# Optimization experiments

Hardware: AMD Instinct MI355X
Metric: run time of the kernel (lower is better)

Reference implementation:

```python
import jax, jax.numpy as jnp
import numpy as np

HID = 16

def _lrconv(x, edge_index, edge_attr, w1, b1, w2, b2):
    # flow='target_to_source': x_i = x[edge_index[0]], x_j = x[edge_index[1]],
    # aggregate (max) at edge_index[0].
    src = edge_index[0]
    dst = edge_index[1]
    m = jnp.concatenate([x[src], x[dst], edge_attr], axis=-1)  # [E, 2*in+edge]
    m = jax.nn.relu(m @ w1 + b1)
    m = jax.nn.relu(m @ w2 + b2)  # [E, out], all >= 0
    agg = jax.ops.segment_max(m, src, num_segments=x.shape[0])
    # empty segments get -inf in jax; PyG fills with 0. Messages are ReLU'd (>=0),
    # so clamping at 0 is exact.
    return jnp.maximum(agg, 0.0)

def _glorot(key, shape):
    fan_in, fan_out = shape
    lim = float(np.sqrt(6.0 / (fan_in + fan_out)))
    return jax.random.uniform(key, shape, jnp.float32, -lim, lim)

def setup_inputs() -> dict:
    key = jax.random.key(0)
    ks = jax.random.split(key, 16)
    N, E = 100000, 1600000
    x = jax.random.normal(ks[0], (N, 4), jnp.float32)
    edge_index = jax.random.randint(ks[1], (2, E), 0, N, jnp.int64)
    edge_attr = jax.random.normal(ks[2], (E, 8), jnp.float32)
    # conv1: in=4 -> cat dim 4*2+8=16
    c1_w1 = _glorot(ks[3], (16, HID)); c1_b1 = jnp.zeros((HID,), jnp.float32)
    c1_w2 = _glorot(ks[4], (HID, 16)); c1_b2 = jnp.zeros((16,), jnp.float32)
    # conv2: in=16 -> cat dim 16*2+8=40
    c2_w1 = _glorot(ks[5], (40, HID)); c2_b1 = jnp.zeros((HID,), jnp.float32)
    c2_w2 = _glorot(ks[6], (HID, 16)); c2_b2 = jnp.zeros((16,), jnp.float32)
    l1_w = _glorot(ks[7], (16, 16)); l1_b = jnp.zeros((16,), jnp.float32)
    l2_w = _glorot(ks[8], (16, 1)); l2_b = jnp.zeros((1,), jnp.float32)
    return {"x": x, "edge_index": edge_index, "edge_attr": edge_attr,
            "c1_w1": c1_w1, "c1_b1": c1_b1, "c1_w2": c1_w2, "c1_b2": c1_b2,
            "c2_w1": c2_w1, "c2_b1": c2_b1, "c2_w2": c2_w2, "c2_b2": c2_b2,
            "l1_w": l1_w, "l1_b": l1_b, "l2_w": l2_w, "l2_b": l2_b}

def reference(x, edge_index, edge_attr,
              c1_w1, c1_b1, c1_w2, c1_b2,
              c2_w1, c2_b1, c2_w2, c2_b2,
              l1_w, l1_b, l2_w, l2_b):
    h = _lrconv(x, edge_index, edge_attr, c1_w1, c1_b1, c1_w2, c1_b2)   # [N,16]
    h = _lrconv(h, edge_index, edge_attr, c2_w1, c2_b1, c2_w2, c2_b2)   # [N,16]
    h = jax.nn.relu(h @ l1_w + l1_b)
    return h @ l2_w + l2_b  # [N,1]
```

## Files before the change

kernel.cpp:

```cpp
#include <hip/hip_runtime.h>
#include <hip/hip_fp16.h>

#define CHUNK 1024
#define NBKT 4

typedef _Float16 half8 __attribute__((ext_vector_type(8)));
typedef float floatx4 __attribute__((ext_vector_type(4)));

__device__ __forceinline__ unsigned int pack2(float a, float b) {
    __half2 h = __floats2half2_rn(a, b);
    return *(unsigned int*)&h;
}
__device__ __forceinline__ float2 unpack2(unsigned int u) {
    __half2 h = *(__half2*)&u;
    return __half22float2(h);
}

__global__ __launch_bounds__(256) void rank_cvt(
    const int* __restrict__ ei, const float* __restrict__ ea,
    int* __restrict__ deg, unsigned short* __restrict__ r,
    _Float16* __restrict__ eah, int E)
{
    int e = blockIdx.x * 256 + threadIdx.x;
    if (e >= E) return;
    int bkt = (e >> 8) & (NBKT - 1);
    r[e] = (unsigned short)atomicAdd(&deg[(size_t)ei[e] * NBKT + bkt], 1);
    float4 a0 = *(const float4*)(ea + (size_t)e * 8);
    float4 a1 = *(const float4*)(ea + (size_t)e * 8 + 4);
    half8 h;
    h[0] = (_Float16)a0.x; h[1] = (_Float16)a0.y;
    h[2] = (_Float16)a0.z; h[3] = (_Float16)a0.w;
    h[4] = (_Float16)a1.x; h[5] = (_Float16)a1.y;
    h[6] = (_Float16)a1.z; h[7] = (_Float16)a1.w;
    *(half8*)(eah + (size_t)e * 8) = h;
}

__global__ __launch_bounds__(256) void scan_chunk_sums(
    const int* __restrict__ v, int* __restrict__ csum, int N)
{
    __shared__ int s[256];
    int base = blockIdx.x * CHUNK;
    int t = threadIdx.x;
    int acc = 0;
    #pragma unroll
    for (int i = 0; i < CHUNK / 256; ++i) {
        int idx = base + t + i * 256;
        if (idx < N) acc += v[idx];
    }
    s[t] = acc; __syncthreads();
    for (int o = 128; o > 0; o >>= 1) {
        if (t < o) s[t] += s[t + o];
        __syncthreads();
    }
    if (t == 0) csum[blockIdx.x] = s[0];
}

__global__ __launch_bounds__(256) void scan_chunk_off(
    const int* __restrict__ csum, int* __restrict__ coff, int nch)
{
    __shared__ int s[256];
    __shared__ int carry;
    int t = threadIdx.x;
    if (t == 0) carry = 0;
    __syncthreads();
    for (int base = 0; base < nch; base += 256) {
        int v = (base + t < nch) ? csum[base + t] : 0;
        s[t] = v; __syncthreads();
        for (int o = 1; o < 256; o <<= 1) {
            int add = (t >= o) ? s[t - o] : 0;
            __syncthreads();
            s[t] += add;
            __syncthreads();
        }
        int excl = carry + (t > 0 ? s[t - 1] : 0);
        if (base + t < nch) coff[base + t] = excl;
        __syncthreads();
        if (t == 0) carry += s[255];
        __syncthreads();
    }
}

__global__ __launch_bounds__(256) void scan_within_excl(
    const int* __restrict__ deg, int* __restrict__ pos,
    const int* __restrict__ coff, int N)
{
    __shared__ int s[256];
    int t = threadIdx.x;
    int base = blockIdx.x * CHUNK + t * 4;
    int v0 = 0, v1 = 0, v2 = 0, v3 = 0;
    if (base + 0 < N) v0 = deg[base + 0];
    if (base + 1 < N) v1 = deg[base + 1];
    if (base + 2 < N) v2 = deg[base + 2];
    if (base + 3 < N) v3 = deg[base + 3];
    s[t] = v0 + v1 + v2 + v3;
    __syncthreads();
    for (int o = 1; o < 256; o <<= 1) {
        int add = (t >= o) ? s[t - o] : 0;
        __syncthreads();
        s[t] += add;
        __syncthreads();
    }
    int run = coff[blockIdx.x] + (t > 0 ? s[t - 1] : 0);
    if (base + 0 < N) pos[base + 0] = run; run += v0;
    if (base + 1 < N) pos[base + 1] = run; run += v1;
    if (base + 2 < N) pos[base + 2] = run; run += v2;
    if (base + 3 < N) pos[base + 3] = run;
}

__global__ __launch_bounds__(256) void edge_mlp1(
    const float* __restrict__ x,
    const int*   __restrict__ ei,
    const _Float16* __restrict__ eah,
    const int*   __restrict__ pos,
    const unsigned short* __restrict__ r,
    const float* __restrict__ w1, const float* __restrict__ b1,
    const float* __restrict__ w2, const float* __restrict__ b2,
    _Float16* __restrict__ m2h,
    int E)
{
    __shared__ _Float16 itm[4][4][16][24];
    int tid = threadIdx.x;
    int w = tid >> 6, lane = tid & 63;
    int e16 = lane & 15, q = lane >> 4;
    int ntiles = (E + 63) >> 6;
    int tile = blockIdx.x * 4 + w;
    if (tile >= ntiles) return;
    int ebase = tile << 6;
    int e = ebase + lane;

    int s_l = 0, d_l = 0, p_l = 0;
    if (e < E) {
        s_l = ei[e];
        d_l = ei[E + e];
        p_l = pos[(size_t)s_l * NBKT + ((e >> 8) & (NBKT - 1))] + (int)r[e];
    }

    half8 B1, B2;
    #pragma unroll
    for (int j = 0; j < 8; ++j) { B1[j] = (_Float16)0.f; B2[j] = (_Float16)0.f; }
    if (q < 2) {
        #pragma unroll
        for (int j = 0; j < 8; ++j) {
            B1[j] = (_Float16)w1[(8 * q + j) * 16 + e16];
            B2[j] = (_Float16)w2[(8 * q + j) * 16 + e16];
        }
    }
    float b1c = b1[e16], b2c = b2[e16];

    half8 A[4];
    #pragma unroll
    for (int t = 0; t < 4; ++t) {
        int st = __shfl(s_l, 16 * t + e16, 64);
        int dt = __shfl(d_l, 16 * t + e16, 64);
        half8 a;
        #pragma unroll
        for (int j = 0; j < 8; ++j) a[j] = (_Float16)0.f;
        int et = ebase + 16 * t + e16;
        if (q == 0 && et < E) {
            float4 xs = *(const float4*)(x + (size_t)st * 4);
            float4 xd = *(const float4*)(x + (size_t)dt * 4);
            a[0] = (_Float16)xs.x; a[1] = (_Float16)xs.y;
            a[2] = (_Float16)xs.z; a[3] = (_Float16)xs.w;
            a[4] = (_Float16)xd.x; a[5] = (_Float16)xd.y;
            a[6] = (_Float16)xd.z; a[7] = (_Float16)xd.w;
        } else if (q == 1 && et < E) {
            a = *(const half8*)(eah + (size_t)et * 8);
        }
        A[t] = a;
    }

    floatx4 C[4];
    #pragma unroll
    for (int t = 0; t < 4; ++t) {
        floatx4 c = {b1c, b1c, b1c, b1c};
        C[t] = __builtin_amdgcn_mfma_f32_16x16x32_f16(A[t], B1, c, 0, 0, 0);
    }
    #pragma unroll
    for (int t = 0; t < 4; ++t)
        #pragma unroll
        for (int i = 0; i < 4; ++i)
            itm[w][t][4 * q + i][e16] = (_Float16)fmaxf(C[t][i], 0.0f);
    __builtin_amdgcn_wave_barrier();

    half8 A2[4];
    #pragma unroll
    for (int t = 0; t < 4; ++t) {
        half8 a;
        #pragma unroll
        for (int j = 0; j < 8; ++j) a[j] = (_Float16)0.f;
        if (q < 2) a = *(const half8*)&itm[w][t][e16][8 * q];
        A2[t] = a;
    }
    __builtin_amdgcn_wave_barrier();
    floatx4 C2[4];
    #pragma unroll
    for (int t = 0; t < 4; ++t) {
        floatx4 c = {b2c, b2c, b2c, b2c};
        C2[t] = __builtin_amdgcn_mfma_f32_16x16x32_f16(A2[t], B2, c, 0, 0, 0);
    }
    #pragma unroll
    for (int t = 0; t < 4; ++t)
        #pragma unroll
        for (int i = 0; i < 4; ++i)
            itm[w][t][4 * q + i][e16] = (_Float16)C2[t][i];
    __builtin_amdgcn_wave_barrier();

    if (e < E) {
        half8 lo = *(const half8*)&itm[w][q][e16][0];
        half8 hi = *(const half8*)&itm[w][q][e16][8];
        *(half8*)(m2h + (size_t)p_l * 16)     = lo;
        *(half8*)(m2h + (size_t)p_l * 16 + 8) = hi;
    }
}

__global__ __launch_bounds__(256) void edge_mlp2(
    const float* __restrict__ hw_s,
    const unsigned short* __restrict__ hw_dh,
    const int*   __restrict__ ei,
    const _Float16* __restrict__ eah,
    const int*   __restrict__ pos,
    const unsigned short* __restrict__ r,
    const float* __restrict__ w1,
    const float* __restrict__ w2, const float* __restrict__ b2,
    _Float16* __restrict__ m2h, int E)
{
    __shared__ _Float16 itm[4][4][16][24];
    int tid = threadIdx.x;
    int w = tid >> 6, lane = tid & 63;
    int e16 = lane & 15, q = lane >> 4;
    const __half* hwd = (const __half*)hw_dh;
    int ntiles = (E + 63) >> 6;
    int tile = blockIdx.x * 4 + w;
    if (tile >= ntiles) return;
    int ebase = tile << 6;
    int e = ebase + lane;

    int s_l = 0, d_l = 0, p_l = 0;
    if (e < E) {
        s_l = ei[e];
        d_l = ei[E + e];
        p_l = pos[(size_t)s_l * NBKT + ((e >> 8) & (NBKT - 1))] + (int)r[e];
    }

    half8 B1, B2;
    #pragma unroll
    for (int j = 0; j < 8; ++j) { B1[j] = (_Float16)0.f; B2[j] = (_Float16)0.f; }
    if (q == 0) {
        #pragma unroll
        for (int j = 0; j < 8; ++j)
            B1[j] = (_Float16)w1[(32 + j) * 16 + e16];
    }
    if (q < 2) {
        #pragma unroll
        for (int j = 0; j < 8; ++j)
            B2[j] = (_Float16)w2[(8 * q + j) * 16 + e16];
    }
    float b2c = b2[e16];

    half8 A[4];
    #pragma unroll
    for (int t = 0; t < 4; ++t) {
        half8 a;
        #pragma unroll
        for (int j = 0; j < 8; ++j) a[j] = (_Float16)0.f;
        int et = ebase + 16 * t + e16;
        if (q == 0 && et < E)
            a = *(const half8*)(eah + (size_t)et * 8);
        A[t] = a;
    }

    floatx4 C[4];
    #pragma unroll
    for (int t = 0; t < 4; ++t) {
        floatx4 c;
        #pragma unroll
        for (int i = 0; i < 4; ++i) {
            int li = 16 * t + 4 * q + i;
            int s = __shfl(s_l, li, 64);
            int d = __shfl(d_l, li, 64);
            int rr = ebase + li;
            float v = 0.0f;
            if (rr < E) {
                v = hw_s[(size_t)s * 16 + e16]
                  + __half2float(hwd[(size_t)d * 16 + e16]);
            }
            c[i] = v;
        }
        C[t] = __builtin_amdgcn_mfma_f32_16x16x32_f16(A[t], B1, c, 0, 0, 0);
    }
    #pragma unroll
    for (int t = 0; t < 4; ++t)
        #pragma unroll
        for (int i = 0; i < 4; ++i)
            itm[w][t][4 * q + i][e16] = (_Float16)fmaxf(C[t][i], 0.0f);
    __builtin_amdgcn_wave_barrier();

    half8 A2[4];
    #pragma unroll
    for (int t = 0; t < 4; ++t) {
        half8 a;
        #pragma unroll
        for (int j = 0; j < 8; ++j) a[j] = (_Float16)0.f;
        if (q < 2) a = *(const half8*)&itm[w][t][e16][8 * q];
        A2[t] = a;
    }
    __builtin_amdgcn_wave_barrier();
    floatx4 C2[4];
    #pragma unroll
    for (int t = 0; t < 4; ++t) {
        floatx4 c = {b2c, b2c, b2c, b2c};
        C2[t] = __builtin_amdgcn_mfma_f32_16x16x32_f16(A2[t], B2, c, 0, 0, 0);
    }
    #pragma unroll
    for (int t = 0; t < 4; ++t)
        #pragma unroll
        for (int i = 0; i < 4; ++i)
            itm[w][t][4 * q + i][e16] = (_Float16)C2[t][i];
    __builtin_amdgcn_wave_barrier();

    if (e < E) {
        half8 lo = *(const half8*)&itm[w][q][e16][0];
        half8 hi = *(const half8*)&itm[w][q][e16][8];
        *(half8*)(m2h + (size_t)p_l * 16)     = lo;
        *(half8*)(m2h + (size_t)p_l * 16 + 8) = hi;
    }
}

__global__ __launch_bounds__(256) void segmax1_hw(
    const _Float16* __restrict__ m2h, const int* __restrict__ pos,
    const float* __restrict__ cw1, const float* __restrict__ cb1,
    float* __restrict__ hw_s, unsigned short* __restrict__ hw_dh,
    int N, int E)
{
    int tid = threadIdx.x;
    int n = blockIdx.x * 32 + (tid >> 3);
    if (n >= N) return;
    int g = tid & 7;
    int start = pos[(size_t)n * NBKT];
    int end = (n + 1 < N) ? pos[(size_t)(n + 1) * NBKT] : E;

    float acc[16];
    #pragma unroll
    for (int j = 0; j < 16; ++j) acc[j] = 0.0f;

    for (int k = start + g; k < end; k += 8) {
        uint4 u0 = *(const uint4*)(m2h + (size_t)k * 16);
        uint4 u1 = *(const uint4*)(m2h + (size_t)k * 16 + 8);
        float2 f;
        f = unpack2(u0.x); acc[0]  = fmaxf(acc[0],  f.x); acc[1]  = fmaxf(acc[1],  f.y);
        f = unpack2(u0.y); acc[2]  = fmaxf(acc[2],  f.x); acc[3]  = fmaxf(acc[3],  f.y);
        f = unpack2(u0.z); acc[4]  = fmaxf(acc[4],  f.x); acc[5]  = fmaxf(acc[5],  f.y);
        f = unpack2(u0.w); acc[6]  = fmaxf(acc[6],  f.x); acc[7]  = fmaxf(acc[7],  f.y);
        f = unpack2(u1.x); acc[8]  = fmaxf(acc[8],  f.x); acc[9]  = fmaxf(acc[9],  f.y);
        f = unpack2(u1.y); acc[10] = fmaxf(acc[10], f.x); acc[11] = fmaxf(acc[11], f.y);
        f = unpack2(u1.z); acc[12] = fmaxf(acc[12], f.x); acc[13] = fmaxf(acc[13], f.y);
        f = unpack2(u1.w); acc[14] = fmaxf(acc[14], f.x); acc[15] = fmaxf(acc[15], f.y);
    }
    #pragma unroll
    for (int mask = 1; mask < 8; mask <<= 1) {
        #pragma unroll
        for (int j = 0; j < 16; ++j)
            acc[j] = fmaxf(acc[j], __shfl_xor(acc[j], mask, 64));
    }

    int j0 = 2 * g, j1 = 2 * g + 1;
    float hs0 = cb1[j0], hs1 = cb1[j1], hd0 = 0.0f, hd1 = 0.0f;
    #pragma unroll
    for (int k = 0; k < 16; ++k) {
        float ak = acc[k];
        hs0 = fmaf(ak, cw1[k * 16 + j0], hs0);
        hs1 = fmaf(ak, cw1[k * 16 + j1], hs1);
        hd0 = fmaf(ak, cw1[(16 + k) * 16 + j0], hd0);
        hd1 = fmaf(ak, cw1[(16 + k) * 16 + j1], hd1);
    }
    *(float2*)(hw_s + (size_t)n * 16 + j0) = make_float2(hs0, hs1);
    ((unsigned int*)hw_dh)[(size_t)n * 8 + g] = pack2(hd0, hd1);
}

__global__ __launch_bounds__(256) void segmax2_head(
    const _Float16* __restrict__ m2h, const int* __restrict__ pos,
    const float* __restrict__ l1w, const float* __restrict__ l1b,
    const float* __restrict__ l2w, const float* __restrict__ l2b,
    float* __restrict__ out, int N, int E)
{
    int tid = threadIdx.x;
    int n = blockIdx.x * 32 + (tid >> 3);
    if (n >= N) return;
    int g = tid & 7;
    int start = pos[(size_t)n * NBKT];
    int end = (n + 1 < N) ? pos[(size_t)(n + 1) * NBKT] : E;

    float acc[16];
    #pragma unroll
    for (int j = 0; j < 16; ++j) acc[j] = 0.0f;

    for (int k = start + g; k < end; k += 8) {
        uint4 u0 = *(const uint4*)(m2h + (size_t)k * 16);
        uint4 u1 = *(const uint4*)(m2h + (size_t)k * 16 + 8);
        float2 f;
        f = unpack2(u0.x); acc[0]  = fmaxf(acc[0],  f.x); acc[1]  = fmaxf(acc[1],  f.y);
        f = unpack2(u0.y); acc[2]  = fmaxf(acc[2],  f.x); acc[3]  = fmaxf(acc[3],  f.y);
        f = unpack2(u0.z); acc[4]  = fmaxf(acc[4],  f.x); acc[5]  = fmaxf(acc[5],  f.y);
        f = unpack2(u0.w); acc[6]  = fmaxf(acc[6],  f.x); acc[7]  = fmaxf(acc[7],  f.y);
        f = unpack2(u1.x); acc[8]  = fmaxf(acc[8],  f.x); acc[9]  = fmaxf(acc[9],  f.y);
        f = unpack2(u1.y); acc[10] = fmaxf(acc[10], f.x); acc[11] = fmaxf(acc[11], f.y);
        f = unpack2(u1.z); acc[12] = fmaxf(acc[12], f.x); acc[13] = fmaxf(acc[13], f.y);
        f = unpack2(u1.w); acc[14] = fmaxf(acc[14], f.x); acc[15] = fmaxf(acc[15], f.y);
    }
    #pragma unroll
    for (int mask = 1; mask < 8; mask <<= 1) {
        #pragma unroll
        for (int j = 0; j < 16; ++j)
            acc[j] = fmaxf(acc[j], __shfl_xor(acc[j], mask, 64));
    }

    float t2[16];
    #pragma unroll
    for (int j = 0; j < 16; ++j) t2[j] = l1b[j];
    #pragma unroll
    for (int kk = 0; kk < 16; ++kk) {
        float ak = acc[kk];
        #pragma unroll
        for (int j = 0; j < 16; ++j) t2[j] = fmaf(ak, l1w[kk * 16 + j], t2[j]);
    }
    float r2 = l2b[0];
    #pragma unroll
    for (int j = 0; j < 16; ++j) r2 = fmaf(fmaxf(t2[j], 0.0f), l2w[j], r2);
    if (g == 0) out[n] = r2;
}

extern "C" void kernel_launch(void* const* d_in, const int* in_sizes, int n_in,
                              void* d_out, int out_size, void* d_ws, size_t ws_size,
                              hipStream_t stream)
{
    const float* x     = (const float*)d_in[0];
    const int*   ei    = (const int*)  d_in[1];
    const float* ea    = (const float*)d_in[2];
    const float* c1_w1 = (const float*)d_in[3];
    const float* c1_b1 = (const float*)d_in[4];
    const float* c1_w2 = (const float*)d_in[5];
    const float* c1_b2 = (const float*)d_in[6];
    const float* c2_w1 = (const float*)d_in[7];
    const float* c2_b1 = (const float*)d_in[8];
    const float* c2_w2 = (const float*)d_in[9];
    const float* c2_b2 = (const float*)d_in[10];
    const float* l1_w  = (const float*)d_in[11];
    const float* l1_b  = (const float*)d_in[12];
    const float* l2_w  = (const float*)d_in[13];
    const float* l2_b  = (const float*)d_in[14];
    float* out = (float*)d_out;

    const int N = in_sizes[0] / 4;
    const int E = in_sizes[2] / 8;
    const int M = N * NBKT;
    const int nch = (M + CHUNK - 1) / CHUNK;

    const int BLK = 256;
    const int egrid = (E + BLK - 1) / BLK;
    const int ggrid = (N + 31) / 32;
    const int ntiles64 = (E + 63) >> 6;
    const int mgrid = (ntiles64 + 3) / 4;

    size_t szN16f = (size_t)N * 16 * 4;
    size_t szN16h = (size_t)N * 16 * 2;
    size_t szPos  = ((size_t)M * 4 + 15) & ~(size_t)15;
    size_t szEh   = ((size_t)E * 2 + 15) & ~(size_t)15;
    size_t szE16  = (size_t)E * 16;

    size_t pos_off  = 0;
    size_t r_off    = pos_off  + szPos;
    size_t hws_off  = r_off    + szEh;
    size_t hwdh_off = hws_off  + szN16f;
    size_t eah_off  = hwdh_off + szN16h;
    size_t m2h_off  = eah_off  + szE16;
    size_t deg_off  = m2h_off;
    size_t cs_off   = deg_off  + szPos;
    size_t cf_off   = cs_off   + 16384;

    int*            pos  = (int*)  ((char*)d_ws + pos_off);
    unsigned short* r    = (unsigned short*)((char*)d_ws + r_off);
    float*          hw_s = (float*)((char*)d_ws + hws_off);
    unsigned short* hwdh = (unsigned short*)((char*)d_ws + hwdh_off);
    _Float16*       eah  = (_Float16*)((char*)d_ws + eah_off);
    _Float16*       m2h  = (_Float16*)((char*)d_ws + m2h_off);
    int*            deg  = (int*)  ((char*)d_ws + deg_off);
    int*            csum = (int*)  ((char*)d_ws + cs_off);
    int*            coff = (int*)  ((char*)d_ws + cf_off);

    hipMemsetAsync(deg, 0, (size_t)M * 4, stream);
    rank_cvt<<<egrid, BLK, 0, stream>>>(ei, ea, deg, r, eah, E);
    scan_chunk_sums<<<nch, BLK, 0, stream>>>(deg, csum, M);
    scan_chunk_off<<<1, 256, 0, stream>>>(csum, coff, nch);
    scan_within_excl<<<nch, BLK, 0, stream>>>(deg, pos, coff, M);
    edge_mlp1<<<mgrid, BLK, 0, stream>>>(x, ei, eah, pos, r,
                                         c1_w1, c1_b1, c1_w2, c1_b2, m2h, E);
    segmax1_hw<<<ggrid, BLK, 0, stream>>>(m2h, pos, c2_w1, c2_b1,
                                          hw_s, hwdh, N, E);
    edge_mlp2<<<mgrid, BLK, 0, stream>>>(hw_s, hwdh, ei, eah, pos, r,
                                         c2_w1, c2_w2, c2_b2, m2h, E);
    segmax2_head<<<ggrid, BLK, 0, stream>>>(m2h, pos, l1_w, l1_b, l2_w, l2_b,
                                            out, N, E);
}
```

Before: 363.1 us.

## Gather fp16 node features in edge MLP2, use packed half max, widen buckets

The second conv no longer precomputes per-node projections (hw_s fp32 plus hw_dh fp16) in the segment-max kernel. Instead, segmax1 writes the fp16 aggregated features h1, and edge_mlp2 gathers h1 rows for source and destination and runs an extra MFMA over the full 40-wide input. Segment-max kernels now take a packed fp16 max over half8 vectors instead of unpacking to fp32. x is pre-converted to fp16 inside rank_cvt, and the atomic bucket count rises from 4 to 8 to spread contention. Gathered bytes per edge go down (32B fp16 versus 64B fp32 plus 32B fp16), at the cost of one more MFMA per tile and a larger pos array.

```diff
diff --git a/kernel.cpp b/kernel.cpp
--- a/kernel.cpp
+++ b/kernel.cpp
@@ -2,29 +2,35 @@
 #include <hip/hip_fp16.h>
 
 #define CHUNK 1024
-#define NBKT 4
+#define NBKT 8
 
 typedef _Float16 half8 __attribute__((ext_vector_type(8)));
+typedef _Float16 half4 __attribute__((ext_vector_type(4)));
 typedef float floatx4 __attribute__((ext_vector_type(4)));
 
-__device__ __forceinline__ unsigned int pack2(float a, float b) {
-    __half2 h = __floats2half2_rn(a, b);
-    return *(unsigned int*)&h;
-}
-__device__ __forceinline__ float2 unpack2(unsigned int u) {
-    __half2 h = *(__half2*)&u;
-    return __half22float2(h);
+union H8 { half8 h; unsigned int u[4]; };
+
+__device__ __forceinline__ half8 hmax8(half8 a, half8 b) {
+#if __has_builtin(__builtin_elementwise_max)
+    return __builtin_elementwise_max(a, b);
+#else
+    half8 r;
+    #pragma unroll
+    for (int j = 0; j < 8; ++j) r[j] = a[j] > b[j] ? a[j] : b[j];
+    return r;
+#endif
 }
 
 __global__ __launch_bounds__(256) void rank_cvt(
     const int* __restrict__ ei, const float* __restrict__ ea,
+    const float* __restrict__ x,
     int* __restrict__ deg, unsigned short* __restrict__ r,
-    _Float16* __restrict__ eah, int E)
+    _Float16* __restrict__ eah, _Float16* __restrict__ xh,
+    int E, int N)
 {
     int e = blockIdx.x * 256 + threadIdx.x;
     if (e >= E) return;
-    int bkt = (e >> 8) & (NBKT - 1);
-    r[e] = (unsigned short)atomicAdd(&deg[(size_t)ei[e] * NBKT + bkt], 1);
+    r[e] = (unsigned short)atomicAdd(&deg[(size_t)ei[e] * NBKT + ((e >> 8) & (NBKT - 1))], 1);
     float4 a0 = *(const float4*)(ea + (size_t)e * 8);
     float4 a1 = *(const float4*)(ea + (size_t)e * 8 + 4);
     half8 h;
@@ -33,6 +39,13 @@
     h[4] = (_Float16)a1.x; h[5] = (_Float16)a1.y;
     h[6] = (_Float16)a1.z; h[7] = (_Float16)a1.w;
     *(half8*)(eah + (size_t)e * 8) = h;
+    if (e < N) {
+        float4 xv = *(const float4*)(x + (size_t)e * 4);
+        half4 hx;
+        hx[0] = (_Float16)xv.x; hx[1] = (_Float16)xv.y;
+        hx[2] = (_Float16)xv.z; hx[3] = (_Float16)xv.w;
+        *(half4*)(xh + (size_t)e * 4) = hx;
+    }
 }
 
 __global__ __launch_bounds__(256) void scan_chunk_sums(
@@ -108,7 +121,7 @@
 }
 
 __global__ __launch_bounds__(256) void edge_mlp1(
-    const float* __restrict__ x,
+    const _Float16* __restrict__ xh,
     const int*   __restrict__ ei,
     const _Float16* __restrict__ eah,
     const int*   __restrict__ pos,
@@ -122,10 +135,8 @@
     int tid = threadIdx.x;
     int w = tid >> 6, lane = tid & 63;
     int e16 = lane & 15, q = lane >> 4;
-    int ntiles = (E + 63) >> 6;
-    int tile = blockIdx.x * 4 + w;
-    if (tile >= ntiles) return;
-    int ebase = tile << 6;
+    int ebase = (blockIdx.x * 4 + w) << 6;
+    if (ebase >= E) return;
     int e = ebase + lane;
 
     int s_l = 0, d_l = 0, p_l = 0;
@@ -157,12 +168,10 @@
         for (int j = 0; j < 8; ++j) a[j] = (_Float16)0.f;
         int et = ebase + 16 * t + e16;
         if (q == 0 && et < E) {
-            float4 xs = *(const float4*)(x + (size_t)st * 4);
-            float4 xd = *(const float4*)(x + (size_t)dt * 4);
-            a[0] = (_Float16)xs.x; a[1] = (_Float16)xs.y;
-            a[2] = (_Float16)xs.z; a[3] = (_Float16)xs.w;
-            a[4] = (_Float16)xd.x; a[5] = (_Float16)xd.y;
-            a[6] = (_Float16)xd.z; a[7] = (_Float16)xd.w;
+            half4 hs = *(const half4*)(xh + (size_t)st * 4);
+            half4 hd = *(const half4*)(xh + (size_t)dt * 4);
+            a[0] = hs[0]; a[1] = hs[1]; a[2] = hs[2]; a[3] = hs[3];
+            a[4] = hd[0]; a[5] = hd[1]; a[6] = hd[2]; a[7] = hd[3];
         } else if (q == 1 && et < E) {
             a = *(const half8*)(eah + (size_t)et * 8);
         }
@@ -214,13 +223,12 @@
 }
 
 __global__ __launch_bounds__(256) void edge_mlp2(
-    const float* __restrict__ hw_s,
-    const unsigned short* __restrict__ hw_dh,
+    const _Float16* __restrict__ h1,
     const int*   __restrict__ ei,
     const _Float16* __restrict__ eah,
     const int*   __restrict__ pos,
     const unsigned short* __restrict__ r,
-    const float* __restrict__ w1,
+    const float* __restrict__ w1, const float* __restrict__ b1v,
     const float* __restrict__ w2, const float* __restrict__ b2,
     _Float16* __restrict__ m2h, int E)
 {
@@ -228,11 +236,8 @@
     int tid = threadIdx.x;
     int w = tid >> 6, lane = tid & 63;
     int e16 = lane & 15, q = lane >> 4;
-    const __half* hwd = (const __half*)hw_dh;
-    int ntiles = (E + 63) >> 6;
-    int tile = blockIdx.x * 4 + w;
-    if (tile >= ntiles) return;
-    int ebase = tile << 6;
+    int ebase = (blockIdx.x * 4 + w) << 6;
+    if (ebase >= E) return;
     int e = ebase + lane;
 
     int s_l = 0, d_l = 0, p_l = 0;
@@ -242,22 +247,25 @@
         p_l = pos[(size_t)s_l * NBKT + ((e >> 8) & (NBKT - 1))] + (int)r[e];
     }
 
-    half8 B1, B2;
-    #pragma unroll
-    for (int j = 0; j < 8; ++j) { B1[j] = (_Float16)0.f; B2[j] = (_Float16)0.f; }
+    half8 B1, B2e, BL2;
+    #pragma unroll
+    for (int j = 0; j < 8; ++j) {
+        B1[j] = (_Float16)w1[(8 * q + j) * 16 + e16];
+        B2e[j] = (_Float16)0.f; BL2[j] = (_Float16)0.f;
+    }
     if (q == 0) {
         #pragma unroll
         for (int j = 0; j < 8; ++j)
-            B1[j] = (_Float16)w1[(32 + j) * 16 + e16];
+            B2e[j] = (_Float16)w1[(32 + j) * 16 + e16];
     }
     if (q < 2) {
         #pragma unroll
         for (int j = 0; j < 8; ++j)
-            B2[j] = (_Float16)w2[(8 * q + j) * 16 + e16];
-    }
-    float b2c = b2[e16];
-
-    half8 A[4];
+            BL2[j] = (_Float16)w2[(8 * q + j) * 16 + e16];
+    }
+    float b1c = b1v[e16], b2c = b2[e16];
+
+    half8 A2[4];
     #pragma unroll
     for (int t = 0; t < 4; ++t) {
         half8 a;
@@ -266,27 +274,24 @@
         int et = ebase + 16 * t + e16;
         if (q == 0 && et < E)
             a = *(const half8*)(eah + (size_t)et * 8);
-        A[t] = a;
+        A2[t] = a;
+    }
+
+    half8 A1[4];
+    #pragma unroll
+    for (int t = 0; t < 4; ++t) {
+        int st = __shfl(s_l, 16 * t + e16, 64);
+        int dt = __shfl(d_l, 16 * t + e16, 64);
+        int row = (q < 2) ? st : dt;
+        A1[t] = *(const half8*)(h1 + (size_t)row * 16 + 8 * (q & 1));
     }
 
     floatx4 C[4];
     #pragma unroll
     for (int t = 0; t < 4; ++t) {
-        floatx4 c;
-        #pragma unroll
-        for (int i = 0; i < 4; ++i) {
-            int li = 16 * t + 4 * q + i;
-            int s = __shfl(s_l, li, 64);
-            int d = __shfl(d_l, li, 64);
-            int rr = ebase + li;
-            float v = 0.0f;
-            if (rr < E) {
-                v = hw_s[(size_t)s * 16 + e16]
-                  + __half2float(hwd[(size_t)d * 16 + e16]);
-            }
-            c[i] = v;
-        }
-        C[t] = __builtin_amdgcn_mfma_f32_16x16x32_f16(A[t], B1, c, 0, 0, 0);
+        floatx4 c = {b1c, b1c, b1c, b1c};
+        c = __builtin_amdgcn_mfma_f32_16x16x32_f16(A2[t], B2e, c, 0, 0, 0);
+        C[t] = __builtin_amdgcn_mfma_f32_16x16x32_f16(A1[t], B1, c, 0, 0, 0);
     }
     #pragma unroll
     for (int t = 0; t < 4; ++t)
@@ -295,21 +300,21 @@
             itm[w][t][4 * q + i][e16] = (_Float16)fmaxf(C[t][i], 0.0f);
     __builtin_amdgcn_wave_barrier();
 
-    half8 A2[4];
+    half8 A2L[4];
     #pragma unroll
     for (int t = 0; t < 4; ++t) {
         half8 a;
         #pragma unroll
         for (int j = 0; j < 8; ++j) a[j] = (_Float16)0.f;
         if (q < 2) a = *(const half8*)&itm[w][t][e16][8 * q];
-        A2[t] = a;
+        A2L[t] = a;
     }
     __builtin_amdgcn_wave_barrier();
     floatx4 C2[4];
     #pragma unroll
     for (int t = 0; t < 4; ++t) {
         floatx4 c = {b2c, b2c, b2c, b2c};
-        C2[t] = __builtin_amdgcn_mfma_f32_16x16x32_f16(A2[t], B2, c, 0, 0, 0);
+        C2[t] = __builtin_amdgcn_mfma_f32_16x16x32_f16(A2L[t], BL2, c, 0, 0, 0);
     }
     #pragma unroll
     for (int t = 0; t < 4; ++t)
@@ -326,10 +331,9 @@
     }
 }
 
-__global__ __launch_bounds__(256) void segmax1_hw(
+__global__ __launch_bounds__(256) void segmax1_h(
     const _Float16* __restrict__ m2h, const int* __restrict__ pos,
-    const float* __restrict__ cw1, const float* __restrict__ cb1,
-    float* __restrict__ hw_s, unsigned short* __restrict__ hw_dh,
+    unsigned int* __restrict__ h1u,
     int N, int E)
 {
     int tid = threadIdx.x;
@@ -339,42 +343,31 @@
     int start = pos[(size_t)n * NBKT];
     int end = (n + 1 < N) ? pos[(size_t)(n + 1) * NBKT] : E;
 
-    float acc[16];
-    #pragma unroll
-    for (int j = 0; j < 16; ++j) acc[j] = 0.0f;
+    half8 a0, a1;
+    #pragma unroll
+    for (int j = 0; j < 8; ++j) { a0[j] = (_Float16)0.f; a1[j] = (_Float16)0.f; }
 
     for (int k = start + g; k < end; k += 8) {
-        uint4 u0 = *(const uint4*)(m2h + (size_t)k * 16);
-        uint4 u1 = *(const uint4*)(m2h + (size_t)k * 16 + 8);
-        float2 f;
-        f = unpack2(u0.x); acc[0]  = fmaxf(acc[0],  f.x); acc[1]  = fmaxf(acc[1],  f.y);
-        f = unpack2(u0.y); acc[2]  = fmaxf(acc[2],  f.x); acc[3]  = fmaxf(acc[3],  f.y);
-        f = unpack2(u0.z); acc[4]  = fmaxf(acc[4],  f.x); acc[5]  = fmaxf(acc[5],  f.y);
-        f = unpack2(u0.w); acc[6]  = fmaxf(acc[6],  f.x); acc[7]  = fmaxf(acc[7],  f.y);
-        f = unpack2(u1.x); acc[8]  = fmaxf(acc[8],  f.x); acc[9]  = fmaxf(acc[9],  f.y);
-        f = unpack2(u1.y); acc[10] = fmaxf(acc[10], f.x); acc[11] = fmaxf(acc[11], f.y);
-        f = unpack2(u1.z); acc[12] = fmaxf(acc[12], f.x); acc[13] = fmaxf(acc[13], f.y);
-        f = unpack2(u1.w); acc[14] = fmaxf(acc[14], f.x); acc[15] = fmaxf(acc[15], f.y);
+        half8 v0 = *(const half8*)(m2h + (size_t)k * 16);
+        half8 v1 = *(const half8*)(m2h + (size_t)k * 16 + 8);
+        a0 = hmax8(a0, v0);
+        a1 = hmax8(a1, v1);
     }
     #pragma unroll
     for (int mask = 1; mask < 8; mask <<= 1) {
-        #pragma unroll
-        for (int j = 0; j < 16; ++j)
-            acc[j] = fmaxf(acc[j], __shfl_xor(acc[j], mask, 64));
-    }
-
-    int j0 = 2 * g, j1 = 2 * g + 1;
-    float hs0 = cb1[j0], hs1 = cb1[j1], hd0 = 0.0f, hd1 = 0.0f;
-    #pragma unroll
-    for (int k = 0; k < 16; ++k) {
-        float ak = acc[k];
-        hs0 = fmaf(ak, cw1[k * 16 + j0], hs0);
-        hs1 = fmaf(ak, cw1[k * 16 + j1], hs1);
-        hd0 = fmaf(ak, cw1[(16 + k) * 16 + j0], hd0);
-        hd1 = fmaf(ak, cw1[(16 + k) * 16 + j1], hd1);
-    }
-    *(float2*)(hw_s + (size_t)n * 16 + j0) = make_float2(hs0, hs1);
-    ((unsigned int*)hw_dh)[(size_t)n * 8 + g] = pack2(hd0, hd1);
+        H8 x0, x1, y0, y1;
+        x0.h = a0; x1.h = a1;
+        #pragma unroll
+        for (int j = 0; j < 4; ++j) {
+            y0.u[j] = __shfl_xor(x0.u[j], mask, 64);
+            y1.u[j] = __shfl_xor(x1.u[j], mask, 64);
+        }
+        a0 = hmax8(a0, y0.h);
+        a1 = hmax8(a1, y1.h);
+    }
+    H8 U0, U1; U0.h = a0; U1.h = a1;
+    unsigned int word = (g < 4) ? U0.u[g & 3] : U1.u[g & 3];
+    h1u[(size_t)n * 8 + g] = word;
 }
 
 __global__ __launch_bounds__(256) void segmax2_head(
@@ -390,29 +383,32 @@
     int start = pos[(size_t)n * NBKT];
     int end = (n + 1 < N) ? pos[(size_t)(n + 1) * NBKT] : E;
 
+    half8 a0, a1;
+    #pragma unroll
+    for (int j = 0; j < 8; ++j) { a0[j] = (_Float16)0.f; a1[j] = (_Float16)0.f; }
+
+    for (int k = start + g; k < end; k += 8) {
+        half8 v0 = *(const half8*)(m2h + (size_t)k * 16);
+        half8 v1 = *(const half8*)(m2h + (size_t)k * 16 + 8);
+        a0 = hmax8(a0, v0);
+        a1 = hmax8(a1, v1);
+    }
+    #pragma unroll
+    for (int mask = 1; mask < 8; mask <<= 1) {
+        H8 x0, x1, y0, y1;
+        x0.h = a0; x1.h = a1;
+        #pragma unroll
+        for (int j = 0; j < 4; ++j) {
+            y0.u[j] = __shfl_xor(x0.u[j], mask, 64);
+            y1.u[j] = __shfl_xor(x1.u[j], mask, 64);
+        }
+        a0 = hmax8(a0, y0.h);
+        a1 = hmax8(a1, y1.h);
+    }
+
     float acc[16];
     #pragma unroll
-    for (int j = 0; j < 16; ++j) acc[j] = 0.0f;
-
-    for (int k = start + g; k < end; k += 8) {
-        uint4 u0 = *(const uint4*)(m2h + (size_t)k * 16);
-        uint4 u1 = *(const uint4*)(m2h + (size_t)k * 16 + 8);
-        float2 f;
-        f = unpack2(u0.x); acc[0]  = fmaxf(acc[0],  f.x); acc[1]  = fmaxf(acc[1],  f.y);
-        f = unpack2(u0.y); acc[2]  = fmaxf(acc[2],  f.x); acc[3]  = fmaxf(acc[3],  f.y);
-        f = unpack2(u0.z); acc[4]  = fmaxf(acc[4],  f.x); acc[5]  = fmaxf(acc[5],  f.y);
-        f = unpack2(u0.w); acc[6]  = fmaxf(acc[6],  f.x); acc[7]  = fmaxf(acc[7],  f.y);
-        f = unpack2(u1.x); acc[8]  = fmaxf(acc[8],  f.x); acc[9]  = fmaxf(acc[9],  f.y);
-        f = unpack2(u1.y); acc[10] = fmaxf(acc[10], f.x); acc[11] = fmaxf(acc[11], f.y);
-        f = unpack2(u1.z); acc[12] = fmaxf(acc[12], f.x); acc[13] = fmaxf(acc[13], f.y);
-        f = unpack2(u1.w); acc[14] = fmaxf(acc[14], f.x); acc[15] = fmaxf(acc[15], f.y);
-    }
-    #pragma unroll
-    for (int mask = 1; mask < 8; mask <<= 1) {
-        #pragma unroll
-        for (int j = 0; j < 16; ++j)
-            acc[j] = fmaxf(acc[j], __shfl_xor(acc[j], mask, 64));
-    }
+    for (int j = 0; j < 8; ++j) { acc[j] = (float)a0[j]; acc[8 + j] = (float)a1[j]; }
 
     float t2[16];
     #pragma unroll
@@ -461,26 +457,27 @@
     const int ntiles64 = (E + 63) >> 6;
     const int mgrid = (ntiles64 + 3) / 4;
 
-    size_t szN16f = (size_t)N * 16 * 4;
-    size_t szN16h = (size_t)N * 16 * 2;
-    size_t szPos  = ((size_t)M * 4 + 15) & ~(size_t)15;
-    size_t szEh   = ((size_t)E * 2 + 15) & ~(size_t)15;
-    size_t szE16  = (size_t)E * 16;
-
-    size_t pos_off  = 0;
-    size_t r_off    = pos_off  + szPos;
-    size_t hws_off  = r_off    + szEh;
-    size_t hwdh_off = hws_off  + szN16f;
-    size_t eah_off  = hwdh_off + szN16h;
-    size_t m2h_off  = eah_off  + szE16;
-    size_t deg_off  = m2h_off;
-    size_t cs_off   = deg_off  + szPos;
-    size_t cf_off   = cs_off   + 16384;
+    size_t szPos = ((size_t)M * 4 + 15) & ~(size_t)15;
+    size_t szR   = ((size_t)E * 2 + 15) & ~(size_t)15;
+    size_t szXh  = ((size_t)N * 8 + 15) & ~(size_t)15;
+    size_t szH1  = ((size_t)N * 32 + 15) & ~(size_t)15;
+    size_t szEah = (size_t)E * 16;
+    size_t szM2h = (size_t)E * 32;
+
+    size_t pos_off = 0;
+    size_t r_off   = pos_off + szPos;
+    size_t xh_off  = r_off   + szR;
+    size_t h1_off  = xh_off  + szXh;
+    size_t eah_off = h1_off  + szH1;
+    size_t m2h_off = eah_off + szEah;
+    size_t deg_off = m2h_off;
+    size_t cs_off  = deg_off + szPos;
+    size_t cf_off  = cs_off + 16384;
 
     int*            pos  = (int*)  ((char*)d_ws + pos_off);
     unsigned short* r    = (unsigned short*)((char*)d_ws + r_off);
-    float*          hw_s = (float*)((char*)d_ws + hws_off);
-    unsigned short* hwdh = (unsigned short*)((char*)d_ws + hwdh_off);
+    _Float16*       xh   = (_Float16*)((char*)d_ws + xh_off);
+    _Float16*       h1   = (_Float16*)((char*)d_ws + h1_off);
     _Float16*       eah  = (_Float16*)((char*)d_ws + eah_off);
     _Float16*       m2h  = (_Float16*)((char*)d_ws + m2h_off);
     int*            deg  = (int*)  ((char*)d_ws + deg_off);
@@ -488,16 +485,15 @@
     int*            coff = (int*)  ((char*)d_ws + cf_off);
 
     hipMemsetAsync(deg, 0, (size_t)M * 4, stream);
-    rank_cvt<<<egrid, BLK, 0, stream>>>(ei, ea, deg, r, eah, E);
+    rank_cvt<<<egrid, BLK, 0, stream>>>(ei, ea, x, deg, r, eah, xh, E, N);
     scan_chunk_sums<<<nch, BLK, 0, stream>>>(deg, csum, M);
     scan_chunk_off<<<1, 256, 0, stream>>>(csum, coff, nch);
     scan_within_excl<<<nch, BLK, 0, stream>>>(deg, pos, coff, M);
-    edge_mlp1<<<mgrid, BLK, 0, stream>>>(x, ei, eah, pos, r,
+    edge_mlp1<<<mgrid, BLK, 0, stream>>>(xh, ei, eah, pos, r,
                                          c1_w1, c1_b1, c1_w2, c1_b2, m2h, E);
-    segmax1_hw<<<ggrid, BLK, 0, stream>>>(m2h, pos, c2_w1, c2_b1,
-                                          hw_s, hwdh, N, E);
-    edge_mlp2<<<mgrid, BLK, 0, stream>>>(hw_s, hwdh, ei, eah, pos, r,
-                                         c2_w1, c2_w2, c2_b2, m2h, E);
+    segmax1_h<<<ggrid, BLK, 0, stream>>>(m2h, pos, (unsigned int*)h1, N, E);
+    edge_mlp2<<<mgrid, BLK, 0, stream>>>(h1, ei, eah, pos, r,
+                                         c2_w1, c2_b1, c2_w2, c2_b2, m2h, E);
     segmax2_head<<<ggrid, BLK, 0, stream>>>(m2h, pos, l1_w, l1_b, l2_w, l2_b,
                                             out, N, E);
 }
```

New measurement: 353.0 us. -2.8%, faster.
